# Kernel tuning notes

Hardware: AMD Instinct MI355X
Metric: run time of the kernel (lower is better)

Reference implementation:

```python
import jax, jax.numpy as jnp
import numpy as np

N_NODES = 100000
N_EDGES = 1600000
IN_DIM = 256
HEADS = 4
OUT_DIM = 32
NEG_SLOPE = 0.2


def setup_inputs() -> dict:
    key = jax.random.key(0)
    ks = jax.random.split(key, 6)
    x = jax.random.normal(ks[0], (N_NODES, IN_DIM), dtype=jnp.float32)
    # xavier-ish init scale for fc and attention vectors
    W = jax.random.normal(ks[1], (IN_DIM, HEADS * OUT_DIM), dtype=jnp.float32) * (1.0 / np.sqrt(IN_DIM))
    attn_l = jax.random.normal(ks[2], (HEADS, OUT_DIM), dtype=jnp.float32) * (1.0 / np.sqrt(OUT_DIM))
    attn_r = jax.random.normal(ks[3], (HEADS, OUT_DIM), dtype=jnp.float32) * (1.0 / np.sqrt(OUT_DIM))
    src = jax.random.randint(ks[4], (N_EDGES,), 0, N_NODES, dtype=jnp.int32)
    dst = jax.random.randint(ks[5], (N_EDGES,), 0, N_NODES, dtype=jnp.int32)
    return {"x": x, "W": W, "attn_l": attn_l, "attn_r": attn_r, "src": src, "dst": dst}


def reference(x, W, attn_l, attn_r, src, dst):
    N = x.shape[0]
    H, D = attn_l.shape
    # shared linear projection (feat_drop = 0)
    feat = (x @ W).reshape(N, H, D)                      # [N,H,D]
    el = jnp.sum(feat * attn_l, axis=-1)                 # [N,H]
    er = jnp.sum(feat * attn_r, axis=-1)                 # [N,H]
    e = jax.nn.leaky_relu(el[src] + er[dst], NEG_SLOPE)  # [E,H]
    # edge softmax over incoming edges of each destination node
    m = jax.ops.segment_max(e, dst, num_segments=N)      # [N,H]
    m = jnp.where(jnp.isfinite(m), m, 0.0)               # zero-in-degree guard
    ex = jnp.exp(e - m[dst])                             # [E,H]
    denom = jax.ops.segment_sum(ex, dst, num_segments=N) # [N,H]
    a = ex / jnp.maximum(denom[dst], 1e-9)               # [E,H] (attn_drop = 0)
    # weighted scatter-add aggregation
    out = jax.ops.segment_sum(a[:, :, None] * feat[src], dst, num_segments=N)  # [N,H,D]
    # head mean (the .mean(1) in GAT1.forward)
    return out.mean(axis=1)                              # [N,D]
```

## Files before the change

kernel.cpp:

```cpp
#include <hip/hip_runtime.h>
#include <math.h>

#define NN 100000
#define NE 1600000
#define IN_DIM 256
#define HD 128
#define NEG_SLOPE 0.2f

#define B1SH 9
#define NPB (1 << B1SH)
#define NB1 ((NN + NPB - 1) / NPB)
#define SC_BLOCKS ((NE / 4 + 1023) / 1024)

typedef __attribute__((ext_vector_type(8))) __bf16 bf16x8;
typedef __attribute__((ext_vector_type(4))) float floatx4;
typedef __attribute__((ext_vector_type(2))) float f32x2;

__device__ inline unsigned short f2bf(float f) {
    unsigned int b = __float_as_uint(f);
    b += 0x7fffu + ((b >> 16) & 1u);
    return (unsigned short)(b >> 16);
}
__device__ inline unsigned int pk(float lo, float hi) {
    return (unsigned int)f2bf(lo) | ((unsigned int)f2bf(hi) << 16);
}
__device__ inline float lrelu(float v) { return (v > 0.f) ? v : v * NEG_SLOPE; }
__device__ inline f32x2 un2(unsigned int v) {
    f32x2 r;
    r.x = __uint_as_float(v << 16);
    r.y = __uint_as_float(v & 0xffff0000u);
    return r;
}

__global__ __launch_bounds__(256) void prep_w_kernel(const float* __restrict__ W,
                                                     unsigned int* __restrict__ wswz) {
    int g = blockIdx.x * 256 + threadIdx.x;
    int lane = g & 63;
    int t = (g >> 6) & 7;
    int c = g >> 9;
    int sub = lane & 15, quad = lane >> 4;
    int n = t * 16 + sub;
    int kbase = c * 32 + quad * 8;
    unsigned int ob = (unsigned int)g * 4;
#pragma unroll
    for (int i = 0; i < 4; ++i) {
        float lo = W[(size_t)(kbase + 2 * i) * HD + n];
        float hi = W[(size_t)(kbase + 2 * i + 1) * HD + n];
        wswz[ob + i] = pk(lo, hi);
    }
}

__global__ __launch_bounds__(256) void gemm_kernel(const float* __restrict__ x,
                                                   const uint4* __restrict__ wswz,
                                                   const float* __restrict__ attn_l,
                                                   const float* __restrict__ attn_r,
                                                   unsigned short* __restrict__ featb,
                                                   float* __restrict__ el,
                                                   float* __restrict__ er) {
    const int tid = threadIdx.x;
    const int lane = tid & 63, wv = tid >> 6;
    const int sub = lane & 15, quad = lane >> 4;
    const int row0 = blockIdx.x * 64 + wv * 16;

    int m = row0 + sub;
    if (m >= NN) m = NN - 1;
    const float* xp = x + (size_t)m * IN_DIM + quad * 8;

    bf16x8 af[8];
#pragma unroll
    for (int h = 0; h < 2; ++h) {
        float4 raw[4][2];
#pragma unroll
        for (int c = 0; c < 4; ++c) {
            raw[c][0] = *(const float4*)(xp + (h * 4 + c) * 32);
            raw[c][1] = *(const float4*)(xp + (h * 4 + c) * 32 + 4);
        }
#pragma unroll
        for (int c = 0; c < 4; ++c) {
            uint4 au;
            au.x = pk(raw[c][0].x, raw[c][0].y);
            au.y = pk(raw[c][0].z, raw[c][0].w);
            au.z = pk(raw[c][1].x, raw[c][1].y);
            au.w = pk(raw[c][1].z, raw[c][1].w);
            af[h * 4 + c] = __builtin_bit_cast(bf16x8, au);
        }
    }

    floatx4 acc[8];
#pragma unroll
    for (int t = 0; t < 8; ++t) acc[t] = (floatx4){0.f, 0.f, 0.f, 0.f};

#pragma unroll
    for (int c = 0; c < 8; ++c) {
        uint4 bu[8];
#pragma unroll
        for (int t = 0; t < 8; ++t) bu[t] = wswz[(c * 8 + t) * 64 + lane];
#pragma unroll
        for (int t = 0; t < 8; ++t) {
            bf16x8 bfr = __builtin_bit_cast(bf16x8, bu[t]);
            acc[t] = __builtin_amdgcn_mfma_f32_16x16x32_bf16(af[c], bfr, acc[t], 0, 0, 0);
        }
    }

    float al[8], ar[8];
#pragma unroll
    for (int t = 0; t < 8; ++t) {
        al[t] = attn_l[t * 16 + sub];
        ar[t] = attn_r[t * 16 + sub];
    }

#pragma unroll
    for (int r = 0; r < 4; ++r) {
        int row = row0 + quad * 4 + r;
        uint4 fv;
        fv.x = pk(acc[0][r], acc[1][r]);
        fv.y = pk(acc[2][r], acc[3][r]);
        fv.z = pk(acc[4][r], acc[5][r]);
        fv.w = pk(acc[6][r], acc[7][r]);
        float pl[4], pr[4];
#pragma unroll
        for (int hh = 0; hh < 4; ++hh) {
            pl[hh] = acc[2 * hh][r] * al[2 * hh] + acc[2 * hh + 1][r] * al[2 * hh + 1];
            pr[hh] = acc[2 * hh][r] * ar[2 * hh] + acc[2 * hh + 1][r] * ar[2 * hh + 1];
        }
#pragma unroll
        for (int o = 1; o < 16; o <<= 1) {
#pragma unroll
            for (int hh = 0; hh < 4; ++hh) {
                pl[hh] += __shfl_xor(pl[hh], o);
                pr[hh] += __shfl_xor(pr[hh], o);
            }
        }
        if (row < NN) {
            *(uint4*)(featb + (size_t)row * HD + sub * 8) = fv;
            if (sub < 4) {
                float vl = (sub == 0) ? pl[0] : (sub == 1) ? pl[1] : (sub == 2) ? pl[2] : pl[3];
                float vr = (sub == 0) ? pr[0] : (sub == 1) ? pr[1] : (sub == 2) ? pr[2] : pr[3];
                el[row * 4 + sub] = vl;
                er[row * 4 + sub] = vr;
            }
        }
    }
}

__global__ __launch_bounds__(256) void precount_kernel(const int4* __restrict__ dst4,
                                                       int* __restrict__ gbcnt) {
    __shared__ int cnt[NB1];
    int t = threadIdx.x;
    for (int i = t; i < NB1; i += 256) cnt[i] = 0;
    __syncthreads();
    int base4 = blockIdx.x * 1024;
#pragma unroll
    for (int k = 0; k < 4; ++k) {
        int gi = base4 + k * 256 + t;
        if (gi < NE / 4) {
            int4 d = dst4[gi];
            atomicAdd(&cnt[d.x >> B1SH], 1);
            atomicAdd(&cnt[d.y >> B1SH], 1);
            atomicAdd(&cnt[d.z >> B1SH], 1);
            atomicAdd(&cnt[d.w >> B1SH], 1);
        }
    }
    __syncthreads();
    for (int i = t; i < NB1; i += 256)
        if (cnt[i]) atomicAdd(&gbcnt[i], cnt[i]);
}

__global__ __launch_bounds__(256) void bscan_kernel(const int* __restrict__ gbcnt,
                                                    int* __restrict__ regstart,
                                                    int* __restrict__ gcursor,
                                                    int* __restrict__ offs) {
    __shared__ int sh[256];
    int t = threadIdx.x;
    int v = (t < NB1) ? gbcnt[t] : 0;
    sh[t] = v;
    __syncthreads();
    for (int o = 1; o < 256; o <<= 1) {
        int a = (t >= o) ? sh[t - o] : 0;
        __syncthreads();
        sh[t] += a;
        __syncthreads();
    }
    int excl = sh[t] - v;
    if (t < NB1) {
        regstart[t] = excl;
        gcursor[t] = excl;
    }
    if (t == 0) {
        regstart[NB1] = NE;
        offs[NN] = NE;
    }
}

__global__ __launch_bounds__(256) void scatter_kernel(const int4* __restrict__ src4,
                                                      const int4* __restrict__ dst4,
                                                      int* __restrict__ gcursor,
                                                      unsigned int* __restrict__ pkd) {
    __shared__ int cnt[NB1];
    __shared__ int gbase[NB1];
    int t = threadIdx.x;
    for (int i = t; i < NB1; i += 256) cnt[i] = 0;
    __syncthreads();

    int base4 = blockIdx.x * 1024;
    unsigned int pkv[16];
    unsigned int brk[16];
#pragma unroll
    for (int k = 0; k < 4; ++k) {
        int gi = base4 + k * 256 + t;
        bool ok = gi < NE / 4;
        int gic = ok ? gi : 0;
        int4 s = src4[gic];
        int4 d = dst4[gic];
        int dd[4] = {d.x, d.y, d.z, d.w};
        int ss[4] = {s.x, s.y, s.z, s.w};
#pragma unroll
        for (int j4 = 0; j4 < 4; ++j4) {
            int e = k * 4 + j4;
            if (ok) {
                int b = dd[j4] >> B1SH;
                int r = atomicAdd(&cnt[b], 1);
                brk[e] = ((unsigned int)b << 12) | (unsigned int)r;
                pkv[e] = ((unsigned int)(dd[j4] & (NPB - 1)) << 17) | (unsigned int)ss[j4];
            } else {
                brk[e] = 0xFFFFFFFFu;
            }
        }
    }
    __syncthreads();
    for (int i = t; i < NB1; i += 256)
        gbase[i] = cnt[i] ? atomicAdd(&gcursor[i], cnt[i]) : 0;
    __syncthreads();
#pragma unroll
    for (int e = 0; e < 16; ++e) {
        if (brk[e] != 0xFFFFFFFFu) {
            int b = brk[e] >> 12;
            int r = brk[e] & 0xFFF;
            pkd[gbase[b] + r] = pkv[e];
        }
    }
}

__global__ __launch_bounds__(256) void build_kernel(const unsigned int* __restrict__ pkd,
                                                    const int* __restrict__ regstart,
                                                    int* __restrict__ offs,
                                                    int* __restrict__ csr_src) {
    __shared__ int fcnt[NPB];
    __shared__ int foffs[NPB];
    __shared__ int ssc[256];
    int b = blockIdx.x, t = threadIdx.x;
    int rs = regstart[b], re = regstart[b + 1];
    int n = re - rs;

    for (int i = t; i < NPB; i += 256) fcnt[i] = 0;
    __syncthreads();
    for (int i = t; i < n; i += 256) {
        unsigned int v = pkd[rs + i];
        atomicAdd(&fcnt[v >> 17], 1);
    }
    __syncthreads();
    int a0 = fcnt[2 * t], a1 = fcnt[2 * t + 1];
    int s = a0 + a1;
    ssc[t] = s;
    __syncthreads();
    for (int o = 1; o < 256; o <<= 1) {
        int u = (t >= o) ? ssc[t - o] : 0;
        __syncthreads();
        ssc[t] += u;
        __syncthreads();
    }
    int excl = ssc[t] - s;
    foffs[2 * t] = excl;
    foffs[2 * t + 1] = excl + a0;
    __syncthreads();
#pragma unroll
    for (int q = 0; q < 2; ++q) {
        int j = t + q * 256;
        int node = b * NPB + j;
        if (node < NN) offs[node] = rs + foffs[j];
    }
    for (int i = t; i < NPB; i += 256) fcnt[i] = 0;
    __syncthreads();
    int i = t;
    for (; i + 768 < n; i += 1024) {
        unsigned int v0 = pkd[rs + i];
        unsigned int v1 = pkd[rs + i + 256];
        unsigned int v2 = pkd[rs + i + 512];
        unsigned int v3 = pkd[rs + i + 768];
        int j0 = v0 >> 17, j1 = v1 >> 17, j2 = v2 >> 17, j3 = v3 >> 17;
        int r0 = atomicAdd(&fcnt[j0], 1);
        int r1 = atomicAdd(&fcnt[j1], 1);
        int r2 = atomicAdd(&fcnt[j2], 1);
        int r3 = atomicAdd(&fcnt[j3], 1);
        csr_src[rs + foffs[j0] + r0] = (int)(v0 & 0x1FFFFu);
        csr_src[rs + foffs[j1] + r1] = (int)(v1 & 0x1FFFFu);
        csr_src[rs + foffs[j2] + r2] = (int)(v2 & 0x1FFFFu);
        csr_src[rs + foffs[j3] + r3] = (int)(v3 & 0x1FFFFu);
    }
    for (; i < n; i += 256) {
        unsigned int v = pkd[rs + i];
        int j = v >> 17;
        int r = atomicAdd(&fcnt[j], 1);
        csr_src[rs + foffs[j] + r] = (int)(v & 0x1FFFFu);
    }
}

#define CH 32
__global__ __launch_bounds__(256, 4) void aggregate_kernel(const uint4* __restrict__ featu4,
                                                           const float4* __restrict__ el4,
                                                           const float4* __restrict__ er4,
                                                           const int* __restrict__ offs,
                                                           const int* __restrict__ csr_src,
                                                           float* __restrict__ out) {
    __shared__ int    s_sv[4][4][CH + 1];
    __shared__ float4 s_a4[4][4][CH + 1];
    __shared__ int sdeg[16], smap[16];

    const int tid = threadIdx.x;
    const int lane = tid & 63, wv = tid >> 6;
    const int g = lane >> 4, sub = lane & 15;

    if (tid < 16) {
        int n0 = blockIdx.x * 16 + tid;
        sdeg[tid] = offs[n0 + 1] - offs[n0];
    }
    __syncthreads();
    if (tid < 16) {
        int d = sdeg[tid];
        int rank = 0;
#pragma unroll
        for (int j = 0; j < 16; ++j) {
            int dj = sdeg[j];
            rank += (dj < d) || (dj == d && j < tid);
        }
        smap[rank] = blockIdx.x * 16 + tid;
    }
    __syncthreads();
    const int node = smap[wv * 4 + g];
    const int beg = offs[node], end = offs[node + 1];

    const float4 erv = er4[node];
    float4 sm = make_float4(0.f, 0.f, 0.f, 0.f);
    f32x2 acc2[4];
#pragma unroll
    for (int i = 0; i < 4; ++i) acc2[i] = (f32x2){0.f, 0.f};

    for (int c0 = beg; c0 < end; c0 += CH) {
        int cnt = end - c0;
        if (cnt > CH) cnt = CH;

        int svr[2];
#pragma unroll
        for (int t = 0; t < 2; ++t) {
            int slot = sub + t * 16;
            int sv = (slot < cnt) ? csr_src[c0 + slot] : 0;
            svr[t] = sv;
            s_sv[wv][g][slot] = sv * 16;
        }

        uint4 ua[8], ub[8];
#pragma unroll
        for (int e = 0; e < 8; ++e)
            ua[e] = featu4[(size_t)s_sv[wv][g][e] + sub];

#pragma unroll
        for (int t = 0; t < 2; ++t) {
            int slot = sub + t * 16;
            float4 w = make_float4(0.f, 0.f, 0.f, 0.f);
            if (slot < cnt) {
                float4 e = el4[svr[t]];
                w.x = __expf(lrelu(e.x + erv.x));
                w.y = __expf(lrelu(e.y + erv.y));
                w.z = __expf(lrelu(e.z + erv.z));
                w.w = __expf(lrelu(e.w + erv.w));
                sm.x += w.x; sm.y += w.y; sm.z += w.z; sm.w += w.w;
            }
            s_a4[wv][g][slot] = w;
        }

        int rounds = (cnt + 7) >> 3;
        int jr = 0;
        while (true) {
            bool m1 = (jr + 1) < rounds;
            if (m1) {
                int nb = (jr + 1) << 3;
#pragma unroll
                for (int e = 0; e < 8; ++e)
                    ub[e] = featu4[(size_t)s_sv[wv][g][nb + e] + sub];
            }
            {
                int jb = jr << 3;
#pragma unroll
                for (int e = 0; e < 8; ++e) {
                    float4 we = s_a4[wv][g][jb + e];
                    uint4 u = ua[e];
                    f32x2 w0 = {we.x, we.x}, w1 = {we.y, we.y};
                    f32x2 w2 = {we.z, we.z}, w3 = {we.w, we.w};
                    acc2[0] = __builtin_elementwise_fma(w0, un2(u.x), acc2[0]);
                    acc2[1] = __builtin_elementwise_fma(w1, un2(u.y), acc2[1]);
                    acc2[2] = __builtin_elementwise_fma(w2, un2(u.z), acc2[2]);
                    acc2[3] = __builtin_elementwise_fma(w3, un2(u.w), acc2[3]);
                }
            }
            ++jr;
            if (!m1) break;
            bool m2 = (jr + 1) < rounds;
            if (m2) {
                int nb = (jr + 1) << 3;
#pragma unroll
                for (int e = 0; e < 8; ++e)
                    ua[e] = featu4[(size_t)s_sv[wv][g][nb + e] + sub];
            }
            {
                int jb = jr << 3;
#pragma unroll
                for (int e = 0; e < 8; ++e) {
                    float4 we = s_a4[wv][g][jb + e];
                    uint4 u = ub[e];
                    f32x2 w0 = {we.x, we.x}, w1 = {we.y, we.y};
                    f32x2 w2 = {we.z, we.z}, w3 = {we.w, we.w};
                    acc2[0] = __builtin_elementwise_fma(w0, un2(u.x), acc2[0]);
                    acc2[1] = __builtin_elementwise_fma(w1, un2(u.y), acc2[1]);
                    acc2[2] = __builtin_elementwise_fma(w2, un2(u.z), acc2[2]);
                    acc2[3] = __builtin_elementwise_fma(w3, un2(u.w), acc2[3]);
                }
            }
            ++jr;
            if (!m2) break;
        }
    }

#pragma unroll
    for (int o = 1; o < 16; o <<= 1) {
        sm.x += __shfl_xor(sm.x, o);
        sm.y += __shfl_xor(sm.y, o);
        sm.z += __shfl_xor(sm.z, o);
        sm.w += __shfl_xor(sm.w, o);
    }
    float ix = 1.f / fmaxf(sm.x, 1e-9f);
    float iy = 1.f / fmaxf(sm.y, 1e-9f);
    float iz = 1.f / fmaxf(sm.z, 1e-9f);
    float iw = 1.f / fmaxf(sm.w, 1e-9f);
    float ox = 0.25f * (acc2[0].x * ix + acc2[1].x * iy + acc2[2].x * iz + acc2[3].x * iw);
    float oy = 0.25f * (acc2[0].y * ix + acc2[1].y * iy + acc2[2].y * iz + acc2[3].y * iw);
    out[node * 32 + sub]      = ox;
    out[node * 32 + 16 + sub] = oy;
}

extern "C" void kernel_launch(void* const* d_in, const int* in_sizes, int n_in,
                              void* d_out, int out_size, void* d_ws, size_t ws_size,
                              hipStream_t stream) {
    const float* x      = (const float*)d_in[0];
    const float* W      = (const float*)d_in[1];
    const float* attn_l = (const float*)d_in[2];
    const float* attn_r = (const float*)d_in[3];
    const int*   src    = (const int*)d_in[4];
    const int*   dst    = (const int*)d_in[5];
    float* out = (float*)d_out;

    char* p = (char*)d_ws;
    auto alloc = [&](size_t bytes) -> void* {
        void* r = (void*)p;
        p += (bytes + 255) & ~(size_t)255;
        return r;
    };
    unsigned short* featb = (unsigned short*)alloc((size_t)NN * HD * 2);
    unsigned int*   wswz  = (unsigned int*)alloc(4096 * 16);
    float* el      = (float*)alloc((size_t)NN * 4 * 4);
    float* er      = (float*)alloc((size_t)NN * 4 * 4);
    int*   offs    = (int*)alloc((size_t)(NN + 1) * 4);
    unsigned int* pkd = (unsigned int*)alloc((size_t)NE * 4);
    int*   csr     = (int*)alloc((size_t)NE * 4);
    int*   gbcnt   = (int*)alloc((size_t)NB1 * 4);
    int*   regstart= (int*)alloc((size_t)(NB1 + 1) * 4);
    int*   gcursor = (int*)alloc((size_t)NB1 * 4);

    hipMemsetAsync(gbcnt, 0, (size_t)NB1 * 4, stream);

    prep_w_kernel<<<16, 256, 0, stream>>>(W, wswz);
    gemm_kernel<<<(NN + 63) / 64, 256, 0, stream>>>(x, (const uint4*)wswz, attn_l, attn_r,
                                                    featb, el, er);
    precount_kernel<<<SC_BLOCKS, 256, 0, stream>>>((const int4*)dst, gbcnt);
    bscan_kernel<<<1, 256, 0, stream>>>(gbcnt, regstart, gcursor, offs);
    scatter_kernel<<<SC_BLOCKS, 256, 0, stream>>>((const int4*)src, (const int4*)dst,
                                                  gcursor, pkd);
    build_kernel<<<NB1, 256, 0, stream>>>(pkd, regstart, offs, csr);
    aggregate_kernel<<<NN / 16, 256, 0, stream>>>((const uint4*)featb, (const float4*)el,
                                                  (const float4*)er, offs, csr, out);
}
```

Baseline: 301.5 us.

## Merge GEMM and edge-bucketing kernels into two fused launches with per-block count matrix

Replaces the memset, W prep, GEMM, precount, block scan and scatter launches with two kernels. The first kernel pairs the W swizzle with per-block bucket counting, writing a 2D count matrix. The second pairs the GEMM blocks with scatter blocks, and each scatter block derives its own deterministic base offset from column sums and prefixes of that matrix. This removes the global atomic cursors and the serial scan kernel and lets the GEMM overlap with the edge scatter. The cost is that every scatter block redundantly reads a column of SC_BLOCKS counts (about 391 entries per bucket) and runs a block scan.

```diff
diff --git a/kernel.cpp b/kernel.cpp
--- a/kernel.cpp
+++ b/kernel.cpp
@@ -11,6 +11,7 @@
 #define NPB (1 << B1SH)
 #define NB1 ((NN + NPB - 1) / NPB)
 #define SC_BLOCKS ((NE / 4 + 1023) / 1024)
+#define GEMM_BLOCKS ((NN + 63) / 64)
 
 typedef __attribute__((ext_vector_type(8))) __bf16 bf16x8;
 typedef __attribute__((ext_vector_type(4))) float floatx4;
@@ -32,211 +33,207 @@
     return r;
 }
 
-__global__ __launch_bounds__(256) void prep_w_kernel(const float* __restrict__ W,
-                                                     unsigned int* __restrict__ wswz) {
-    int g = blockIdx.x * 256 + threadIdx.x;
-    int lane = g & 63;
-    int t = (g >> 6) & 7;
-    int c = g >> 9;
-    int sub = lane & 15, quad = lane >> 4;
-    int n = t * 16 + sub;
-    int kbase = c * 32 + quad * 8;
-    unsigned int ob = (unsigned int)g * 4;
-#pragma unroll
-    for (int i = 0; i < 4; ++i) {
-        float lo = W[(size_t)(kbase + 2 * i) * HD + n];
-        float hi = W[(size_t)(kbase + 2 * i + 1) * HD + n];
-        wswz[ob + i] = pk(lo, hi);
-    }
-}
-
-__global__ __launch_bounds__(256) void gemm_kernel(const float* __restrict__ x,
-                                                   const uint4* __restrict__ wswz,
-                                                   const float* __restrict__ attn_l,
-                                                   const float* __restrict__ attn_r,
-                                                   unsigned short* __restrict__ featb,
-                                                   float* __restrict__ el,
-                                                   float* __restrict__ er) {
-    const int tid = threadIdx.x;
-    const int lane = tid & 63, wv = tid >> 6;
-    const int sub = lane & 15, quad = lane >> 4;
-    const int row0 = blockIdx.x * 64 + wv * 16;
-
-    int m = row0 + sub;
-    if (m >= NN) m = NN - 1;
-    const float* xp = x + (size_t)m * IN_DIM + quad * 8;
-
-    bf16x8 af[8];
-#pragma unroll
-    for (int h = 0; h < 2; ++h) {
-        float4 raw[4][2];
-#pragma unroll
-        for (int c = 0; c < 4; ++c) {
-            raw[c][0] = *(const float4*)(xp + (h * 4 + c) * 32);
-            raw[c][1] = *(const float4*)(xp + (h * 4 + c) * 32 + 4);
-        }
-#pragma unroll
-        for (int c = 0; c < 4; ++c) {
-            uint4 au;
-            au.x = pk(raw[c][0].x, raw[c][0].y);
-            au.y = pk(raw[c][0].z, raw[c][0].w);
-            au.z = pk(raw[c][1].x, raw[c][1].y);
-            au.w = pk(raw[c][1].z, raw[c][1].w);
-            af[h * 4 + c] = __builtin_bit_cast(bf16x8, au);
-        }
-    }
-
-    floatx4 acc[8];
-#pragma unroll
-    for (int t = 0; t < 8; ++t) acc[t] = (floatx4){0.f, 0.f, 0.f, 0.f};
-
-#pragma unroll
-    for (int c = 0; c < 8; ++c) {
-        uint4 bu[8];
-#pragma unroll
-        for (int t = 0; t < 8; ++t) bu[t] = wswz[(c * 8 + t) * 64 + lane];
-#pragma unroll
-        for (int t = 0; t < 8; ++t) {
-            bf16x8 bfr = __builtin_bit_cast(bf16x8, bu[t]);
-            acc[t] = __builtin_amdgcn_mfma_f32_16x16x32_bf16(af[c], bfr, acc[t], 0, 0, 0);
-        }
-    }
-
-    float al[8], ar[8];
-#pragma unroll
-    for (int t = 0; t < 8; ++t) {
-        al[t] = attn_l[t * 16 + sub];
-        ar[t] = attn_r[t * 16 + sub];
-    }
-
-#pragma unroll
-    for (int r = 0; r < 4; ++r) {
-        int row = row0 + quad * 4 + r;
-        uint4 fv;
-        fv.x = pk(acc[0][r], acc[1][r]);
-        fv.y = pk(acc[2][r], acc[3][r]);
-        fv.z = pk(acc[4][r], acc[5][r]);
-        fv.w = pk(acc[6][r], acc[7][r]);
-        float pl[4], pr[4];
-#pragma unroll
-        for (int hh = 0; hh < 4; ++hh) {
-            pl[hh] = acc[2 * hh][r] * al[2 * hh] + acc[2 * hh + 1][r] * al[2 * hh + 1];
-            pr[hh] = acc[2 * hh][r] * ar[2 * hh] + acc[2 * hh + 1][r] * ar[2 * hh + 1];
-        }
-#pragma unroll
-        for (int o = 1; o < 16; o <<= 1) {
-#pragma unroll
-            for (int hh = 0; hh < 4; ++hh) {
-                pl[hh] += __shfl_xor(pl[hh], o);
-                pr[hh] += __shfl_xor(pr[hh], o);
-            }
-        }
-        if (row < NN) {
-            *(uint4*)(featb + (size_t)row * HD + sub * 8) = fv;
-            if (sub < 4) {
-                float vl = (sub == 0) ? pl[0] : (sub == 1) ? pl[1] : (sub == 2) ? pl[2] : pl[3];
-                float vr = (sub == 0) ? pr[0] : (sub == 1) ? pr[1] : (sub == 2) ? pr[2] : pr[3];
-                el[row * 4 + sub] = vl;
-                er[row * 4 + sub] = vr;
-            }
-        }
-    }
-}
-
-__global__ __launch_bounds__(256) void precount_kernel(const int4* __restrict__ dst4,
-                                                       int* __restrict__ gbcnt) {
+__global__ __launch_bounds__(256) void d1_kernel(const float* __restrict__ W,
+                                                 unsigned int* __restrict__ wswz,
+                                                 const int4* __restrict__ dst4,
+                                                 int* __restrict__ gcnt2d) {
     __shared__ int cnt[NB1];
-    int t = threadIdx.x;
-    for (int i = t; i < NB1; i += 256) cnt[i] = 0;
-    __syncthreads();
-    int base4 = blockIdx.x * 1024;
-#pragma unroll
-    for (int k = 0; k < 4; ++k) {
-        int gi = base4 + k * 256 + t;
-        if (gi < NE / 4) {
-            int4 d = dst4[gi];
-            atomicAdd(&cnt[d.x >> B1SH], 1);
-            atomicAdd(&cnt[d.y >> B1SH], 1);
-            atomicAdd(&cnt[d.z >> B1SH], 1);
-            atomicAdd(&cnt[d.w >> B1SH], 1);
-        }
-    }
-    __syncthreads();
-    for (int i = t; i < NB1; i += 256)
-        if (cnt[i]) atomicAdd(&gbcnt[i], cnt[i]);
-}
-
-__global__ __launch_bounds__(256) void bscan_kernel(const int* __restrict__ gbcnt,
-                                                    int* __restrict__ regstart,
-                                                    int* __restrict__ gcursor,
-                                                    int* __restrict__ offs) {
-    __shared__ int sh[256];
-    int t = threadIdx.x;
-    int v = (t < NB1) ? gbcnt[t] : 0;
-    sh[t] = v;
-    __syncthreads();
-    for (int o = 1; o < 256; o <<= 1) {
-        int a = (t >= o) ? sh[t - o] : 0;
-        __syncthreads();
-        sh[t] += a;
-        __syncthreads();
-    }
-    int excl = sh[t] - v;
-    if (t < NB1) {
-        regstart[t] = excl;
-        gcursor[t] = excl;
-    }
-    if (t == 0) {
-        regstart[NB1] = NE;
-        offs[NN] = NE;
-    }
-}
-
-__global__ __launch_bounds__(256) void scatter_kernel(const int4* __restrict__ src4,
-                                                      const int4* __restrict__ dst4,
-                                                      int* __restrict__ gcursor,
-                                                      unsigned int* __restrict__ pkd) {
+    const int t = threadIdx.x;
+    if (blockIdx.x < SC_BLOCKS) {
+        for (int i = t; i < NB1; i += 256) cnt[i] = 0;
+        __syncthreads();
+        int base4 = blockIdx.x * 1024;
+#pragma unroll
+        for (int k = 0; k < 4; ++k) {
+            int gi = base4 + k * 256 + t;
+            if (gi < NE / 4) {
+                int4 d = dst4[gi];
+                atomicAdd(&cnt[d.x >> B1SH], 1);
+                atomicAdd(&cnt[d.y >> B1SH], 1);
+                atomicAdd(&cnt[d.z >> B1SH], 1);
+                atomicAdd(&cnt[d.w >> B1SH], 1);
+            }
+        }
+        __syncthreads();
+        for (int i = t; i < NB1; i += 256)
+            gcnt2d[blockIdx.x * NB1 + i] = cnt[i];
+    } else {
+        int g = (blockIdx.x - SC_BLOCKS) * 256 + t;
+        int lane = g & 63;
+        int tt = (g >> 6) & 7;
+        int c = g >> 9;
+        int sub = lane & 15, quad = lane >> 4;
+        int n = tt * 16 + sub;
+        int kbase = c * 32 + quad * 8;
+        unsigned int ob = (unsigned int)g * 4;
+#pragma unroll
+        for (int i = 0; i < 4; ++i) {
+            float lo = W[(size_t)(kbase + 2 * i) * HD + n];
+            float hi = W[(size_t)(kbase + 2 * i + 1) * HD + n];
+            wswz[ob + i] = pk(lo, hi);
+        }
+    }
+}
+
+__global__ __launch_bounds__(256) void d2_kernel(const float* __restrict__ x,
+                                                 const uint4* __restrict__ wswz,
+                                                 const float* __restrict__ attn_l,
+                                                 const float* __restrict__ attn_r,
+                                                 unsigned short* __restrict__ featb,
+                                                 float* __restrict__ el,
+                                                 float* __restrict__ er,
+                                                 const int4* __restrict__ src4,
+                                                 const int4* __restrict__ dst4,
+                                                 const int* __restrict__ gcnt2d,
+                                                 unsigned int* __restrict__ pkd,
+                                                 int* __restrict__ regstart) {
     __shared__ int cnt[NB1];
     __shared__ int gbase[NB1];
-    int t = threadIdx.x;
-    for (int i = t; i < NB1; i += 256) cnt[i] = 0;
-    __syncthreads();
-
-    int base4 = blockIdx.x * 1024;
-    unsigned int pkv[16];
-    unsigned int brk[16];
-#pragma unroll
-    for (int k = 0; k < 4; ++k) {
-        int gi = base4 + k * 256 + t;
-        bool ok = gi < NE / 4;
-        int gic = ok ? gi : 0;
-        int4 s = src4[gic];
-        int4 d = dst4[gic];
-        int dd[4] = {d.x, d.y, d.z, d.w};
-        int ss[4] = {s.x, s.y, s.z, s.w};
-#pragma unroll
-        for (int j4 = 0; j4 < 4; ++j4) {
-            int e = k * 4 + j4;
-            if (ok) {
-                int b = dd[j4] >> B1SH;
-                int r = atomicAdd(&cnt[b], 1);
-                brk[e] = ((unsigned int)b << 12) | (unsigned int)r;
-                pkv[e] = ((unsigned int)(dd[j4] & (NPB - 1)) << 17) | (unsigned int)ss[j4];
-            } else {
-                brk[e] = 0xFFFFFFFFu;
-            }
-        }
-    }
-    __syncthreads();
-    for (int i = t; i < NB1; i += 256)
-        gbase[i] = cnt[i] ? atomicAdd(&gcursor[i], cnt[i]) : 0;
-    __syncthreads();
-#pragma unroll
-    for (int e = 0; e < 16; ++e) {
-        if (brk[e] != 0xFFFFFFFFu) {
-            int b = brk[e] >> 12;
-            int r = brk[e] & 0xFFF;
-            pkd[gbase[b] + r] = pkv[e];
+    __shared__ int sh[256];
+    const int t = threadIdx.x;
+
+    if (blockIdx.x < SC_BLOCKS) {
+        const int b = blockIdx.x;
+        int colsum = 0, mypre = 0;
+        if (t < NB1) {
+            for (int bb = 0; bb < SC_BLOCKS; ++bb) {
+                int v = gcnt2d[bb * NB1 + t];
+                colsum += v;
+                if (bb < b) mypre += v;
+            }
+        }
+        sh[t] = (t < NB1) ? colsum : 0;
+        __syncthreads();
+        for (int o = 1; o < 256; o <<= 1) {
+            int a = (t >= o) ? sh[t - o] : 0;
+            __syncthreads();
+            sh[t] += a;
+            __syncthreads();
+        }
+        int rstart = sh[t] - ((t < NB1) ? colsum : 0);
+        if (t < NB1) gbase[t] = rstart + mypre;
+        if (b == 0 && t < NB1) regstart[t] = rstart;
+        if (b == 0 && t == 0) regstart[NB1] = NE;
+        for (int i = t; i < NB1; i += 256) cnt[i] = 0;
+        __syncthreads();
+
+        int base4 = b * 1024;
+        unsigned int pkv[16];
+        unsigned int brk[16];
+#pragma unroll
+        for (int k = 0; k < 4; ++k) {
+            int gi = base4 + k * 256 + t;
+            bool ok = gi < NE / 4;
+            int gic = ok ? gi : 0;
+            int4 s = src4[gic];
+            int4 d = dst4[gic];
+            int dd[4] = {d.x, d.y, d.z, d.w};
+            int ss[4] = {s.x, s.y, s.z, s.w};
+#pragma unroll
+            for (int j4 = 0; j4 < 4; ++j4) {
+                int e = k * 4 + j4;
+                if (ok) {
+                    int bk = dd[j4] >> B1SH;
+                    int r = atomicAdd(&cnt[bk], 1);
+                    brk[e] = ((unsigned int)bk << 12) | (unsigned int)r;
+                    pkv[e] = ((unsigned int)(dd[j4] & (NPB - 1)) << 17) | (unsigned int)ss[j4];
+                } else {
+                    brk[e] = 0xFFFFFFFFu;
+                }
+            }
+        }
+        __syncthreads();
+#pragma unroll
+        for (int e = 0; e < 16; ++e) {
+            if (brk[e] != 0xFFFFFFFFu) {
+                int bk = brk[e] >> 12;
+                int r = brk[e] & 0xFFF;
+                pkd[gbase[bk] + r] = pkv[e];
+            }
+        }
+    } else {
+        const int lane = t & 63, wv = t >> 6;
+        const int sub = lane & 15, quad = lane >> 4;
+        const int row0 = (blockIdx.x - SC_BLOCKS) * 64 + wv * 16;
+
+        int m = row0 + sub;
+        if (m >= NN) m = NN - 1;
+        const float* xp = x + (size_t)m * IN_DIM + quad * 8;
+
+        bf16x8 af[8];
+#pragma unroll
+        for (int h = 0; h < 2; ++h) {
+            float4 raw[4][2];
+#pragma unroll
+            for (int c = 0; c < 4; ++c) {
+                raw[c][0] = *(const float4*)(xp + (h * 4 + c) * 32);
+                raw[c][1] = *(const float4*)(xp + (h * 4 + c) * 32 + 4);
+            }
+#pragma unroll
+            for (int c = 0; c < 4; ++c) {
+                uint4 au;
+                au.x = pk(raw[c][0].x, raw[c][0].y);
+                au.y = pk(raw[c][0].z, raw[c][0].w);
+                au.z = pk(raw[c][1].x, raw[c][1].y);
+                au.w = pk(raw[c][1].z, raw[c][1].w);
+                af[h * 4 + c] = __builtin_bit_cast(bf16x8, au);
+            }
+        }
+
+        floatx4 acc[8];
+#pragma unroll
+        for (int tt = 0; tt < 8; ++tt) acc[tt] = (floatx4){0.f, 0.f, 0.f, 0.f};
+
+#pragma unroll
+        for (int c = 0; c < 8; ++c) {
+            uint4 bu[8];
+#pragma unroll
+            for (int tt = 0; tt < 8; ++tt) bu[tt] = wswz[(c * 8 + tt) * 64 + lane];
+#pragma unroll
+            for (int tt = 0; tt < 8; ++tt) {
+                bf16x8 bfr = __builtin_bit_cast(bf16x8, bu[tt]);
+                acc[tt] = __builtin_amdgcn_mfma_f32_16x16x32_bf16(af[c], bfr, acc[tt], 0, 0, 0);
+            }
+        }
+
+        float al[8], ar[8];
+#pragma unroll
+        for (int tt = 0; tt < 8; ++tt) {
+            al[tt] = attn_l[tt * 16 + sub];
+            ar[tt] = attn_r[tt * 16 + sub];
+        }
+
+#pragma unroll
+        for (int r = 0; r < 4; ++r) {
+            int row = row0 + quad * 4 + r;
+            uint4 fv;
+            fv.x = pk(acc[0][r], acc[1][r]);
+            fv.y = pk(acc[2][r], acc[3][r]);
+            fv.z = pk(acc[4][r], acc[5][r]);
+            fv.w = pk(acc[6][r], acc[7][r]);
+            float pl[4], pr[4];
+#pragma unroll
+            for (int hh = 0; hh < 4; ++hh) {
+                pl[hh] = acc[2 * hh][r] * al[2 * hh] + acc[2 * hh + 1][r] * al[2 * hh + 1];
+                pr[hh] = acc[2 * hh][r] * ar[2 * hh] + acc[2 * hh + 1][r] * ar[2 * hh + 1];
+            }
+#pragma unroll
+            for (int o = 1; o < 16; o <<= 1) {
+#pragma unroll
+                for (int hh = 0; hh < 4; ++hh) {
+                    pl[hh] += __shfl_xor(pl[hh], o);
+                    pr[hh] += __shfl_xor(pr[hh], o);
+                }
+            }
+            if (row < NN) {
+                *(uint4*)(featb + (size_t)row * HD + sub * 8) = fv;
+                if (sub < 4) {
+                    float vl = (sub == 0) ? pl[0] : (sub == 1) ? pl[1] : (sub == 2) ? pl[2] : pl[3];
+                    float vr = (sub == 0) ? pr[0] : (sub == 1) ? pr[1] : (sub == 2) ? pr[2] : pr[3];
+                    el[row * 4 + sub] = vl;
+                    er[row * 4 + sub] = vr;
+                }
+            }
         }
     }
 }
@@ -251,6 +248,7 @@
     int b = blockIdx.x, t = threadIdx.x;
     int rs = regstart[b], re = regstart[b + 1];
     int n = re - rs;
+    if (b == 0 && t == 0) offs[NN] = NE;
 
     for (int i = t; i < NPB; i += 256) fcnt[i] = 0;
     __syncthreads();
@@ -471,19 +469,14 @@
     int*   offs    = (int*)alloc((size_t)(NN + 1) * 4);
     unsigned int* pkd = (unsigned int*)alloc((size_t)NE * 4);
     int*   csr     = (int*)alloc((size_t)NE * 4);
-    int*   gbcnt   = (int*)alloc((size_t)NB1 * 4);
+    int*   gcnt2d  = (int*)alloc((size_t)SC_BLOCKS * NB1 * 4);
     int*   regstart= (int*)alloc((size_t)(NB1 + 1) * 4);
-    int*   gcursor = (int*)alloc((size_t)NB1 * 4);
-
-    hipMemsetAsync(gbcnt, 0, (size_t)NB1 * 4, stream);
-
-    prep_w_kernel<<<16, 256, 0, stream>>>(W, wswz);
-    gemm_kernel<<<(NN + 63) / 64, 256, 0, stream>>>(x, (const uint4*)wswz, attn_l, attn_r,
-                                                    featb, el, er);
-    precount_kernel<<<SC_BLOCKS, 256, 0, stream>>>((const int4*)dst, gbcnt);
-    bscan_kernel<<<1, 256, 0, stream>>>(gbcnt, regstart, gcursor, offs);
-    scatter_kernel<<<SC_BLOCKS, 256, 0, stream>>>((const int4*)src, (const int4*)dst,
-                                                  gcursor, pkd);
+
+    d1_kernel<<<SC_BLOCKS + 16, 256, 0, stream>>>(W, wswz, (const int4*)dst, gcnt2d);
+    d2_kernel<<<SC_BLOCKS + GEMM_BLOCKS, 256, 0, stream>>>(x, (const uint4*)wswz, attn_l, attn_r,
+                                                           featb, el, er,
+                                                           (const int4*)src, (const int4*)dst,
+                                                           gcnt2d, pkd, regstart);
     build_kernel<<<NB1, 256, 0, stream>>>(pkd, regstart, offs, csr);
     aggregate_kernel<<<NN / 16, 256, 0, stream>>>((const uint4*)featb, (const float4*)el,
                                                   (const float4*)er, offs, csr, out);
```

Result: faster. 284.5 us (-5.6%).
